# Kernel optimization log

Measured on AMD Instinct MI355X. Metric: run time of the kernel, lower is better.

The kernel has to match this reference:

```python
import jax, jax.numpy as jnp
import numpy as np

B, M, V, E, D, T = 512, 64, 20000, 1024, 384, 100
EPS = 1e-5


def setup_inputs() -> dict:
    key = jax.random.key(0)
    ks = jax.random.split(key, 26)
    w = lambda k, shape: (jax.random.normal(k, shape, jnp.float32) * 0.02)
    return {
        'x': jax.random.uniform(ks[0], (B, V), jnp.float32),
        'emb': jax.random.normal(ks[1], (B, M, D), jnp.float32),
        'lengths': jax.random.randint(ks[2], (B,), 1, M + 1, jnp.int32),
        'fc11_w': w(ks[3], (E, V)), 'fc11_b': jnp.zeros((E,), jnp.float32),
        'fc12_w': w(ks[4], (E, E)), 'fc12_b': jnp.zeros((E,), jnp.float32),
        'q_w': w(ks[5], (D, E)), 'q_b': jnp.zeros((D,), jnp.float32),
        'k_w': w(ks[6], (D, D)), 'k_b': jnp.zeros((D,), jnp.float32),
        'v_w': w(ks[7], (D, D)), 'v_b': jnp.zeros((D,), jnp.float32),
        'mean_w': w(ks[8], (T, D)), 'mean_b': jnp.zeros((T,), jnp.float32),
        'logvar_w': w(ks[9], (T, D)), 'logvar_b': jnp.zeros((T,), jnp.float32),
        'mean_bn_b': jnp.zeros((T,), jnp.float32),
        'logvar_bn_b': jnp.zeros((T,), jnp.float32),
        'dec_w': w(ks[10], (V, T)), 'dec_b': jnp.zeros((V,), jnp.float32),
        'dec_bn_b': jnp.zeros((V,), jnp.float32),
    }


def _bn(h, bias):
    # BatchNorm1d, training-mode batch stats, weight frozen at 1 (requires_grad=False)
    mu = h.mean(axis=0)
    var = h.var(axis=0)  # biased variance, as torch BN normalization
    return (h - mu) / jnp.sqrt(var + EPS) + bias


def reference(x, emb, lengths, fc11_w, fc11_b, fc12_w, fc12_b,
              q_w, q_b, k_w, k_b, v_w, v_b,
              mean_w, mean_b, logvar_w, logvar_b,
              mean_bn_b, logvar_bn_b, dec_w, dec_b, dec_bn_b):
    # encoder MLP (dropout p=0 -> identity)
    e1 = jax.nn.softplus(x @ fc11_w.T + fc11_b)
    h_bow = jax.nn.softplus(e1 @ fc12_w.T + fc12_b)  # [B, E]

    # ragged single-query attention over sentence embeddings, vectorized
    q = h_bow @ q_w.T + q_b                              # [B, D]
    k = jnp.einsum('bmd,ed->bme', emb, k_w) + k_b        # [B, M, D]
    v = jnp.einsum('bmd,ed->bme', emb, v_w) + v_b        # [B, M, D]
    scores = jnp.einsum('bd,bmd->bm', q, k) / jnp.sqrt(jnp.float32(D))
    valid = jnp.arange(M)[None, :] < lengths[:, None]    # [B, M]
    scores = jnp.where(valid, scores, -jnp.inf)
    alpha = jax.nn.softmax(scores, axis=-1)
    d_i = jnp.einsum('bm,bmd->bd', alpha, v)             # [B, D]

    mu = _bn(d_i @ mean_w.T + mean_b, mean_bn_b)         # [B, T]
    logvar = _bn(d_i @ logvar_w.T + logvar_b, logvar_bn_b)
    z = mu  # eval-mode reparameterize
    theta = jax.nn.softmax(z, axis=1)

    logit = theta @ dec_w.T + dec_b
    recon_log = jax.nn.log_softmax(_bn(logit, dec_bn_b), axis=-1)
    recon_loss = -(x * recon_log).sum(axis=1).mean()

    # KL prior: a = ones -> mu2 = 0, var2 = 1 - 1/T (scalar)
    var2 = 1.0 - 1.0 / T
    var = jnp.exp(logvar)
    kld = 0.5 * ((var / var2 + mu * mu / var2 + jnp.log(var2) - logvar).sum(axis=1) - T)
    loss_kl = kld.mean()
    return recon_loss + loss_kl
```

## Files before the change

kernel.cpp:

```cpp
#include <hip/hip_runtime.h>
#include <cstddef>

#define NB 512
#define NM 64
#define NV 20000
#define NE 1024
#define ND 384
#define NT 100
#define EPS 1e-5f

#define NVP 20096
#define NKP 128
#define NHS 256

typedef __bf16 bf16x8 __attribute__((ext_vector_type(8)));
typedef float f32x4 __attribute__((ext_vector_type(4)));

__device__ __forceinline__ float softplus_f(float x) {
    return fmaxf(x, 0.f) + log1pf(expf(-fabsf(x)));
}

__device__ __forceinline__ unsigned short f2bf(float f) {
    unsigned u = __builtin_bit_cast(unsigned, f);
    unsigned r = u + 0x7FFFu + ((u >> 16) & 1u);
    return (unsigned short)(r >> 16);
}

__device__ __forceinline__ float bf2f(unsigned short u) {
    return __builtin_bit_cast(float, (unsigned)u << 16);
}

__device__ __forceinline__ uint4 pack_bf8(float4 a, float4 b) {
    bf16x8 v;
    v[0] = (__bf16)a.x; v[1] = (__bf16)a.y; v[2] = (__bf16)a.z; v[3] = (__bf16)a.w;
    v[4] = (__bf16)b.x; v[5] = (__bf16)b.y; v[6] = (__bf16)b.z; v[7] = (__bf16)b.w;
    return __builtin_bit_cast(uint4, v);
}

__device__ __forceinline__ void convert8(const float* __restrict__ s,
                                         unsigned short* __restrict__ d,
                                         int b, int tid) {
    const size_t i = ((size_t)b * 256 + tid) * 8;
    const float4 a = *reinterpret_cast<const float4*>(s + i);
    const float4 c = *reinterpret_cast<const float4*>(s + i + 4);
    *reinterpret_cast<uint4*>(d + i) = pack_bf8(a, c);
}

#define PREP_C12 512
#define PREP_QW  192
#define PREP_VW  72
#define PREP_TR  144
#define PREP_HD  257
#define PREP_DW  (NVP / 2)
#define PREP_BLOCKS (PREP_C12 + PREP_QW + PREP_VW + PREP_TR + PREP_HD + PREP_DW)

__global__ __launch_bounds__(256) void prep_kernel(
        const float* __restrict__ fc12_w, unsigned short* __restrict__ w12b,
        const float* __restrict__ q_w,    unsigned short* __restrict__ qwb,
        const float* __restrict__ v_w,    unsigned short* __restrict__ vwb,
        const float* __restrict__ k_w,    unsigned short* __restrict__ kTb,
        const float* __restrict__ mw, const float* __restrict__ lw,
        const float* __restrict__ mb, const float* __restrict__ lb,
        unsigned short* __restrict__ headwb, float* __restrict__ headbb,
        const float* __restrict__ dec_w,  unsigned short* __restrict__ decwb) {
    __shared__ float tile[32][33];
    int b = blockIdx.x;
    const int tid = threadIdx.x;
    if (b < PREP_C12) { convert8(fc12_w, w12b, b, tid); return; }
    b -= PREP_C12;
    if (b < PREP_QW) { convert8(q_w, qwb, b, tid); return; }
    b -= PREP_QW;
    if (b < PREP_VW) { convert8(v_w, vwb, b, tid); return; }
    b -= PREP_VW;
    if (b < PREP_TR) {
        const int bx = (b % 12) * 32, by = (b / 12) * 32;
        const int tx = tid & 31, ty = tid >> 5;
        #pragma unroll
        for (int i = 0; i < 4; ++i)
            tile[ty + 8 * i][tx] = k_w[(size_t)(by + ty + 8 * i) * ND + bx + tx];
        __syncthreads();
        #pragma unroll
        for (int i = 0; i < 4; ++i)
            kTb[(size_t)(bx + ty + 8 * i) * ND + by + tx] = f2bf(tile[tx][ty + 8 * i]);
        return;
    }
    b -= PREP_TR;
    if (b < PREP_HD) {
        if (b == NHS) {
            if (tid < NHS)
                headbb[tid] = (tid < NT) ? mb[tid]
                            : (tid >= 128 && tid < 128 + NT) ? lb[tid - 128] : 0.f;
            return;
        }
        const float* src = (b < NT) ? (mw + (size_t)b * ND)
                         : (b >= 128 && b < 128 + NT) ? (lw + (size_t)(b - 128) * ND) : nullptr;
        for (int c = tid; c < ND; c += 256)
            headwb[(size_t)b * ND + c] = src ? f2bf(src[c]) : (unsigned short)0;
        return;
    }
    b -= PREP_HD;
    {
        const int n = b * 2 + (tid >> 7);
        const int k = tid & 127;
        decwb[(size_t)n * NKP + k] =
            (n < NV && k < NT) ? f2bf(dec_w[(size_t)n * NT + k]) : (unsigned short)0;
    }
}

#define BM 128
#define BN 128
#define BK 32

__global__ __launch_bounds__(256) void gemm_f32_splitk(
        const float* __restrict__ A,
        const float* __restrict__ Bw,
        unsigned short* __restrict__ partial,
        int M, int N, int K, int S, int steps_total, int gx, int gy) {
    __shared__ __align__(16) unsigned short Asl[BM * BK];
    __shared__ __align__(16) unsigned short Bsl[BN * BK];
    const int tid = threadIdx.x;
    const int l = blockIdx.x >> 3;
    const int xcd = blockIdx.x & 7;
    const int bm = l % gy;
    const int rest = l / gy;
    const int bn = rest % gx;
    const int s_loc = rest / gx;
    const int s = xcd * (S >> 3) + s_loc;

    const int row0 = bm * BM, col0 = bn * BN;
    const int k_begin = (int)(((long)s * steps_total) / S) * BK;
    const int k_end   = (int)(((long)(s + 1) * steps_total) / S) * BK;
    const int nsteps = (k_end - k_begin) / BK;

    const int sr = tid >> 2;
    const int sc = (tid & 3) * 8;
    const int wave = tid >> 6, lane = tid & 63;
    const int wm = wave >> 1, wn = wave & 1;
    const int lrow = lane & 15, lkb = lane >> 4;

    f32x4 acc[4][4] = {};
    const float* Ab = A + (size_t)row0 * K;
    const float* Bb = Bw + (size_t)col0 * K;

    float4 ra[2][2], rb[2][2];

#define LOADREGS(K0)                                                          \
    {                                                                         \
        _Pragma("unroll")                                                     \
        for (int h = 0; h < 2; ++h) {                                         \
            const float* pa = Ab + (size_t)(h * 64 + sr) * K + (K0) + sc;     \
            const float* pb = Bb + (size_t)(h * 64 + sr) * K + (K0) + sc;     \
            ra[h][0] = *reinterpret_cast<const float4*>(pa);                  \
            ra[h][1] = *reinterpret_cast<const float4*>(pa + 4);              \
            rb[h][0] = *reinterpret_cast<const float4*>(pb);                  \
            rb[h][1] = *reinterpret_cast<const float4*>(pb + 4);              \
        }                                                                     \
    }

#define WRITELDS()                                                            \
    {                                                                         \
        _Pragma("unroll")                                                     \
        for (int h = 0; h < 2; ++h) {                                         \
            *reinterpret_cast<uint4*>(&Asl[(h * 64 + sr) * BK + sc]) =        \
                pack_bf8(ra[h][0], ra[h][1]);                                 \
            *reinterpret_cast<uint4*>(&Bsl[(h * 64 + sr) * BK + sc]) =        \
                pack_bf8(rb[h][0], rb[h][1]);                                 \
        }                                                                     \
    }

    LOADREGS(k_begin);
    WRITELDS();
    __syncthreads();

    for (int t = 0; t < nsteps; ++t) {
        const bool has_next = (t + 1) < nsteps;
        if (has_next) LOADREGS(k_begin + (t + 1) * BK);

        bf16x8 af[4], bfr[4];
        #pragma unroll
        for (int i = 0; i < 4; ++i) {
            af[i]  = *reinterpret_cast<const bf16x8*>(&Asl[(wm * 64 + i * 16 + lrow) * BK + lkb * 8]);
            bfr[i] = *reinterpret_cast<const bf16x8*>(&Bsl[(wn * 64 + i * 16 + lrow) * BK + lkb * 8]);
        }
        #pragma unroll
        for (int i = 0; i < 4; ++i)
            #pragma unroll
            for (int j = 0; j < 4; ++j)
                acc[i][j] = __builtin_amdgcn_mfma_f32_16x16x32_bf16(af[i], bfr[j], acc[i][j], 0, 0, 0);

        __syncthreads();
        if (has_next) WRITELDS();
        __syncthreads();
    }
#undef LOADREGS
#undef WRITELDS

    unsigned short* P = partial + (size_t)s * M * N;
    #pragma unroll
    for (int i = 0; i < 4; ++i) {
        const int rbase = row0 + wm * 64 + i * 16 + lkb * 4;
        #pragma unroll
        for (int j = 0; j < 4; ++j) {
            const int col = col0 + wn * 64 + j * 16 + lrow;
            #pragma unroll
            for (int r = 0; r < 4; ++r)
                P[(size_t)(rbase + r) * N + col] = f2bf(acc[i][j][r]);
        }
    }
}

__global__ __launch_bounds__(256) void gemm_mfma_splitk(
        const unsigned short* __restrict__ A,
        const unsigned short* __restrict__ Bw,
        unsigned short* __restrict__ partial,
        int M, int N, int K, int S, int steps_total) {
    __shared__ __align__(16) unsigned short Asl[BM * BK];
    __shared__ __align__(16) unsigned short Bsl[BN * BK];
    const int tid = threadIdx.x;
    const int bn = blockIdx.x, bm = blockIdx.y, s = blockIdx.z;
    const int row0 = bm * BM, col0 = bn * BN;
    const int k_begin = (int)(((long)s * steps_total) / S) * BK;
    const int k_end   = (int)(((long)(s + 1) * steps_total) / S) * BK;

    const int srow = tid >> 2;
    const int scol = (tid & 3) * 8;
    const int wave = tid >> 6, lane = tid & 63;
    const int wm = wave >> 1, wn = wave & 1;
    const int lrow = lane & 15, lkb = lane >> 4;

    f32x4 acc[4][4] = {};
    const unsigned short* Ab = A + (size_t)row0 * K;
    const unsigned short* Bb = Bw + (size_t)col0 * K;

    for (int k0 = k_begin; k0 < k_end; k0 += BK) {
        #pragma unroll
        for (int i = 0; i < 2; ++i) {
            const int r = i * 64 + srow;
            __builtin_amdgcn_global_load_lds(
                (const __attribute__((address_space(1))) void*)(Ab + (size_t)r * K + k0 + scol),
                (__attribute__((address_space(3))) void*)(&Asl[(i * 256 + tid) * 8]),
                16, 0, 0);
            __builtin_amdgcn_global_load_lds(
                (const __attribute__((address_space(1))) void*)(Bb + (size_t)r * K + k0 + scol),
                (__attribute__((address_space(3))) void*)(&Bsl[(i * 256 + tid) * 8]),
                16, 0, 0);
        }
        __syncthreads();
        bf16x8 af[4], bfr[4];
        #pragma unroll
        for (int i = 0; i < 4; ++i) {
            af[i]  = *reinterpret_cast<const bf16x8*>(&Asl[(wm * 64 + i * 16 + lrow) * BK + lkb * 8]);
            bfr[i] = *reinterpret_cast<const bf16x8*>(&Bsl[(wn * 64 + i * 16 + lrow) * BK + lkb * 8]);
        }
        #pragma unroll
        for (int i = 0; i < 4; ++i)
            #pragma unroll
            for (int j = 0; j < 4; ++j)
                acc[i][j] = __builtin_amdgcn_mfma_f32_16x16x32_bf16(af[i], bfr[j], acc[i][j], 0, 0, 0);
        __syncthreads();
    }

    unsigned short* P = partial + (size_t)s * M * N;
    #pragma unroll
    for (int i = 0; i < 4; ++i) {
        const int rbase = row0 + wm * 64 + i * 16 + lkb * 4;
        #pragma unroll
        for (int j = 0; j < 4; ++j) {
            const int col = col0 + wn * 64 + j * 16 + lrow;
            #pragma unroll
            for (int r = 0; r < 4; ++r)
                P[(size_t)(rbase + r) * N + col] = f2bf(acc[i][j][r]);
        }
    }
}

__global__ __launch_bounds__(256) void gemm64_splitk(
        const unsigned short* __restrict__ A,
        const unsigned short* __restrict__ Bw,
        unsigned short* __restrict__ partial,
        int M, int N, int K, int S, int steps_total) {
    __shared__ __align__(16) unsigned short Asl[64 * BK];
    __shared__ __align__(16) unsigned short Bsl[64 * BK];
    const int tid = threadIdx.x;
    const int bn = blockIdx.x, bm = blockIdx.y, s = blockIdx.z;
    const int row0 = bm * 64, col0 = bn * 64;
    const int k_begin = (int)(((long)s * steps_total) / S) * BK;
    const int k_end   = (int)(((long)(s + 1) * steps_total) / S) * BK;

    const int srow = tid >> 2;
    const int scol = (tid & 3) * 8;
    const int wave = tid >> 6, lane = tid & 63;
    const int wm = wave >> 1, wn = wave & 1;
    const int lrow = lane & 15, lkb = lane >> 4;

    f32x4 acc[2][2] = {};
    const unsigned short* Ab = A + (size_t)row0 * K;
    const unsigned short* Bb = Bw + (size_t)col0 * K;

    for (int k0 = k_begin; k0 < k_end; k0 += BK) {
        __builtin_amdgcn_global_load_lds(
            (const __attribute__((address_space(1))) void*)(Ab + (size_t)srow * K + k0 + scol),
            (__attribute__((address_space(3))) void*)(&Asl[tid * 8]),
            16, 0, 0);
        __builtin_amdgcn_global_load_lds(
            (const __attribute__((address_space(1))) void*)(Bb + (size_t)srow * K + k0 + scol),
            (__attribute__((address_space(3))) void*)(&Bsl[tid * 8]),
            16, 0, 0);
        __syncthreads();
        bf16x8 af[2], bfr[2];
        #pragma unroll
        for (int i = 0; i < 2; ++i) {
            af[i]  = *reinterpret_cast<const bf16x8*>(&Asl[(wm * 32 + i * 16 + lrow) * BK + lkb * 8]);
            bfr[i] = *reinterpret_cast<const bf16x8*>(&Bsl[(wn * 32 + i * 16 + lrow) * BK + lkb * 8]);
        }
        #pragma unroll
        for (int i = 0; i < 2; ++i)
            #pragma unroll
            for (int j = 0; j < 2; ++j)
                acc[i][j] = __builtin_amdgcn_mfma_f32_16x16x32_bf16(af[i], bfr[j], acc[i][j], 0, 0, 0);
        __syncthreads();
    }

    unsigned short* P = partial + (size_t)s * M * N;
    #pragma unroll
    for (int i = 0; i < 2; ++i) {
        const int rbase = row0 + wm * 32 + i * 16 + lkb * 4;
        #pragma unroll
        for (int j = 0; j < 2; ++j) {
            const int col = col0 + wn * 32 + j * 16 + lrow;
            #pragma unroll
            for (int r = 0; r < 4; ++r)
                P[(size_t)(rbase + r) * N + col] = f2bf(acc[i][j][r]);
        }
    }
}

template<int OUT_BF16, int ACT, int HASBIAS>
__global__ __launch_bounds__(256) void reduce_splitk_bf(
        const unsigned short* __restrict__ partial,
        const float* __restrict__ bias,
        void* __restrict__ out, int MN, int N, int S) {
    const int i0 = (blockIdx.x * 256 + threadIdx.x) * 8;
    if (i0 >= MN) return;
    float sum[8] = {};
    for (int s = 0; s < S; ++s) {
        union { uint4 v; unsigned short u[8]; } p;
        p.v = *reinterpret_cast<const uint4*>(partial + (size_t)s * MN + i0);
        #pragma unroll
        for (int j = 0; j < 8; ++j) sum[j] += bf2f(p.u[j]);
    }
    if (HASBIAS) {
        const int nb = i0 % N;
        #pragma unroll
        for (int j = 0; j < 8; ++j) sum[j] += bias[nb + j];
    }
    if (ACT) {
        #pragma unroll
        for (int j = 0; j < 8; ++j) sum[j] = softplus_f(sum[j]);
    }
    if (OUT_BF16) {
        union { uint4 v; unsigned short u[8]; } r;
        #pragma unroll
        for (int j = 0; j < 8; ++j) r.u[j] = f2bf(sum[j]);
        *reinterpret_cast<uint4*>((unsigned short*)out + i0) = r.v;
    } else {
        float* o = (float*)out + i0;
        *reinterpret_cast<float4*>(o)     = make_float4(sum[0], sum[1], sum[2], sum[3]);
        *reinterpret_cast<float4*>(o + 4) = make_float4(sum[4], sum[5], sum[6], sum[7]);
    }
}

template<int OUT_BF16, int ACT, int HASBIAS, int COLSTATS>
__global__ __launch_bounds__(256) void gemm_mfma(
        const unsigned short* __restrict__ A,
        const unsigned short* __restrict__ Bw,
        const float* __restrict__ bias,
        void* __restrict__ Cout,
        float* __restrict__ colp,
        int M, int Nout, int K) {
    __shared__ __align__(16) unsigned short Asl[BM * BK];
    __shared__ __align__(16) unsigned short Bsl[BN * BK];
    const int tid = threadIdx.x;
    const int row0 = blockIdx.y * BM, col0 = blockIdx.x * BN;
    const int srow = tid >> 2;
    const int scol = (tid & 3) * 8;
    const int wave = tid >> 6, lane = tid & 63;
    const int wm = wave >> 1, wn = wave & 1;
    const int lrow = lane & 15, lkb = lane >> 4;

    f32x4 acc[4][4] = {};
    const unsigned short* Ab = A + (size_t)row0 * K;
    const unsigned short* Bb = Bw + (size_t)col0 * K;

    for (int k0 = 0; k0 < K; k0 += BK) {
        #pragma unroll
        for (int i = 0; i < 2; ++i) {
            const int r = i * 64 + srow;
            __builtin_amdgcn_global_load_lds(
                (const __attribute__((address_space(1))) void*)(Ab + (size_t)r * K + k0 + scol),
                (__attribute__((address_space(3))) void*)(&Asl[(i * 256 + tid) * 8]),
                16, 0, 0);
            __builtin_amdgcn_global_load_lds(
                (const __attribute__((address_space(1))) void*)(Bb + (size_t)r * K + k0 + scol),
                (__attribute__((address_space(3))) void*)(&Bsl[(i * 256 + tid) * 8]),
                16, 0, 0);
        }
        __syncthreads();
        bf16x8 af[4], bfr[4];
        #pragma unroll
        for (int i = 0; i < 4; ++i) {
            af[i]  = *reinterpret_cast<const bf16x8*>(&Asl[(wm * 64 + i * 16 + lrow) * BK + lkb * 8]);
            bfr[i] = *reinterpret_cast<const bf16x8*>(&Bsl[(wn * 64 + i * 16 + lrow) * BK + lkb * 8]);
        }
        #pragma unroll
        for (int i = 0; i < 4; ++i)
            #pragma unroll
            for (int j = 0; j < 4; ++j)
                acc[i][j] = __builtin_amdgcn_mfma_f32_16x16x32_bf16(af[i], bfr[j], acc[i][j], 0, 0, 0);
        __syncthreads();
    }

    #pragma unroll
    for (int j = 0; j < 4; ++j) {
        const int col = col0 + wn * 64 + j * 16 + lrow;
        const bool cok = col < Nout;
        const float bv = HASBIAS ? (cok ? bias[col] : 0.f) : 0.f;
        float csum = 0.f, csq = 0.f;
        #pragma unroll
        for (int i = 0; i < 4; ++i) {
            const int rbase = row0 + wm * 64 + i * 16 + lkb * 4;
            #pragma unroll
            for (int r = 0; r < 4; ++r) {
                float v = acc[i][j][r] + bv;
                if (ACT == 1) v = softplus_f(v);
                if (COLSTATS) { csum += v; csq = fmaf(v, v, csq); }
                if (cok) {
                    if (OUT_BF16)
                        ((unsigned short*)Cout)[(size_t)(rbase + r) * Nout + col] = f2bf(v);
                    else
                        ((float*)Cout)[(size_t)(rbase + r) * Nout + col] = v;
                }
            }
        }
        if (COLSTATS) {
            csum += __shfl_xor(csum, 16); csum += __shfl_xor(csum, 32);
            csq  += __shfl_xor(csq, 16);  csq  += __shfl_xor(csq, 32);
            if (lkb == 0) {
                const int w8 = blockIdx.y * 2 + wm;
                colp[(size_t)w8 * NVP + col] = csum;
                colp[(size_t)(8 + w8) * NVP + col] = csq;
            }
        }
    }
}

__global__ __launch_bounds__(256) void attn_kernel(const unsigned short* __restrict__ qkp,
                                                   const float* __restrict__ emb,
                                                   const int* __restrict__ lengths,
                                                   unsigned short* __restrict__ cb) {
    const int b = blockIdx.x;
    const int tid = threadIdx.x;
    __shared__ unsigned short es[NM * ND];
    __shared__ float qs[ND];
    __shared__ float sc[NM];

    const float* ebase = emb + (size_t)b * NM * ND;
    for (int i = tid; i < NM * ND / 8; i += 256) {
        const float4 v0 = *reinterpret_cast<const float4*>(ebase + (size_t)i * 8);
        const float4 v1 = *reinterpret_cast<const float4*>(ebase + (size_t)i * 8 + 4);
        *reinterpret_cast<uint4*>(&es[i * 8]) = pack_bf8(v0, v1);
    }
    for (int d = tid; d < ND; d += 256) {
        float acc = 0.f;
        #pragma unroll
        for (int s = 0; s < 8; ++s)
            acc += bf2f(qkp[((size_t)s * NB + b) * ND + d]);
        qs[d] = acc;
    }
    __syncthreads();

    const int wave = tid >> 6, lane = tid & 63;
    const float scale = 0.05103103630798288f;

    for (int m = wave; m < NM; m += 4) {
        float s = 0.f;
        for (int d = lane; d < ND; d += 64) s = fmaf(bf2f(es[m * ND + d]), qs[d], s);
        #pragma unroll
        for (int off = 32; off; off >>= 1) s += __shfl_xor(s, off);
        if (lane == 0) sc[m] = s * scale;
    }
    __syncthreads();

    const int len = lengths[b];
    if (tid < 64) {
        float s = (tid < len) ? sc[tid] : -INFINITY;
        float mx = s;
        #pragma unroll
        for (int off = 32; off; off >>= 1) mx = fmaxf(mx, __shfl_xor(mx, off));
        float e = (tid < len) ? expf(s - mx) : 0.f;
        float sum = e;
        #pragma unroll
        for (int off = 32; off; off >>= 1) sum += __shfl_xor(sum, off);
        sc[tid] = e / sum;
    }
    __syncthreads();

    for (int d = tid; d < ND; d += 256) {
        float acc = 0.f;
        for (int m = 0; m < len; ++m) acc = fmaf(sc[m], bf2f(es[m * ND + d]), acc);
        cb[(size_t)b * ND + d] = f2bf(acc);
    }
}

__global__ __launch_bounds__(256) void bn_batch(const float* __restrict__ hl,
                                                const float* __restrict__ mbnb,
                                                const float* __restrict__ lbnb,
                                                float* __restrict__ mu,
                                                float* __restrict__ lv) {
    const int t = blockIdx.x;
    const int sel = blockIdx.y;
    const int col = sel ? 128 + t : t;
    const float* bnb = sel ? lbnb : mbnb;
    float* dst = sel ? lv : mu;
    const int tid = threadIdx.x;

    float s = 0.f, ss = 0.f;
    for (int b = tid; b < NB; b += 256) {
        const float v = hl[(size_t)b * NHS + col];
        s += v; ss += v * v;
    }
    __shared__ float rs[256], rss[256];
    rs[tid] = s; rss[tid] = ss;
    __syncthreads();
    for (int off = 128; off; off >>= 1) {
        if (tid < off) { rs[tid] += rs[tid + off]; rss[tid] += rss[tid + off]; }
        __syncthreads();
    }
    const float mean = rs[0] / (float)NB;
    const float var = rss[0] / (float)NB - mean * mean;
    const float rstd = rsqrtf(var + EPS);
    const float bb = bnb[t];
    for (int b = tid; b < NB; b += 256) {
        dst[(size_t)b * NT + t] = (hl[(size_t)b * NHS + col] - mean) * rstd + bb;
    }
}

__global__ __launch_bounds__(128) void theta_kl(const float* __restrict__ mu,
                                                const float* __restrict__ lv,
                                                unsigned short* __restrict__ thetab,
                                                float* __restrict__ kld_p) {
    const int b = blockIdx.x, tid = threadIdx.x;
    const float var2 = 1.0f - 1.0f / (float)NT;
    const float inv_var2 = 1.0f / var2;
    __shared__ float red[128];

    const float m = (tid < NT) ? mu[(size_t)b * NT + tid] : -INFINITY;
    red[tid] = m;
    __syncthreads();
    for (int off = 64; off; off >>= 1) {
        if (tid < off) red[tid] = fmaxf(red[tid], red[tid + off]);
        __syncthreads();
    }
    const float mx = red[0];
    __syncthreads();

    const float e = (tid < NT) ? expf(m - mx) : 0.f;
    red[tid] = e;
    __syncthreads();
    for (int off = 64; off; off >>= 1) {
        if (tid < off) red[tid] += red[tid + off];
        __syncthreads();
    }
    const float sum = red[0];
    __syncthreads();
    thetab[(size_t)b * NKP + tid] = (tid < NT) ? f2bf(e / sum) : (unsigned short)0;

    float term = 0.f;
    if (tid < NT) {
        const float l = lv[(size_t)b * NT + tid];
        term = expf(l) * inv_var2 + m * m * inv_var2 - l;
    }
    red[tid] = term;
    __syncthreads();
    for (int off = 64; off; off >>= 1) {
        if (tid < off) red[tid] += red[tid + off];
        __syncthreads();
    }
    if (tid == 0)
        kld_p[b] = 0.5f * (red[0] + (float)NT * logf(var2) - (float)NT);
}

__global__ __launch_bounds__(256) void stats_final(const float* __restrict__ colp,
                                                   float* __restrict__ cmu,
                                                   float* __restrict__ crstd) {
    const int v = blockIdx.x * 256 + threadIdx.x;
    if (v >= NV) return;
    float s = 0.f, q = 0.f;
    #pragma unroll
    for (int w = 0; w < 8; ++w) {
        s += colp[(size_t)w * NVP + v];
        q += colp[(size_t)(8 + w) * NVP + v];
    }
    const float mean = s / (float)NB;
    cmu[v] = mean;
    crstd[v] = rsqrtf(q / (float)NB - mean * mean + EPS);
}

__global__ __launch_bounds__(256) void row_recon(const unsigned short* __restrict__ logitb,
                                                 const float* __restrict__ x,
                                                 const float* __restrict__ cmu,
                                                 const float* __restrict__ crstd,
                                                 const float* __restrict__ dbnb,
                                                 float* __restrict__ recon_p) {
    const int b = blockIdx.x, tid = threadIdx.x;
    const unsigned short* lr = logitb + (size_t)b * NV;
    const float* xr = x + (size_t)b * NV;

    float m_i = -INFINITY, s_i = 0.f, xz = 0.f, xs = 0.f;
    for (int v = tid * 8; v < NV; v += 2048) {
        union { uint4 v4; unsigned short u[8]; } lw;
        lw.v4 = *reinterpret_cast<const uint4*>(lr + v);
        const float4 x0 = *reinterpret_cast<const float4*>(xr + v);
        const float4 x1 = *reinterpret_cast<const float4*>(xr + v + 4);
        const float4 c0 = *reinterpret_cast<const float4*>(cmu + v);
        const float4 c1 = *reinterpret_cast<const float4*>(cmu + v + 4);
        const float4 r0 = *reinterpret_cast<const float4*>(crstd + v);
        const float4 r1 = *reinterpret_cast<const float4*>(crstd + v + 4);
        const float4 d0 = *reinterpret_cast<const float4*>(dbnb + v);
        const float4 d1 = *reinterpret_cast<const float4*>(dbnb + v + 4);
        const float xv[8] = {x0.x,x0.y,x0.z,x0.w,x1.x,x1.y,x1.z,x1.w};
        const float cm[8] = {c0.x,c0.y,c0.z,c0.w,c1.x,c1.y,c1.z,c1.w};
        const float cr[8] = {r0.x,r0.y,r0.z,r0.w,r1.x,r1.y,r1.z,r1.w};
        const float db[8] = {d0.x,d0.y,d0.z,d0.w,d1.x,d1.y,d1.z,d1.w};
        float z[8];
        #pragma unroll
        for (int j = 0; j < 8; ++j)
            z[j] = fmaf(bf2f(lw.u[j]) - cm[j], cr[j], db[j]);
        float mx = z[0];
        #pragma unroll
        for (int j = 1; j < 8; ++j) mx = fmaxf(mx, z[j]);
        const float mnew = fmaxf(m_i, mx);
        float e8 = 0.f;
        #pragma unroll
        for (int j = 0; j < 8; ++j) e8 += expf(z[j] - mnew);
        s_i = s_i * expf(m_i - mnew) + e8;
        m_i = mnew;
        #pragma unroll
        for (int j = 0; j < 8; ++j) {
            xz = fmaf(xv[j], z[j], xz);
            xs += xv[j];
        }
    }

    __shared__ float rm[256], rs[256], rxz[256], rxs[256];
    rm[tid] = m_i; rs[tid] = s_i; rxz[tid] = xz; rxs[tid] = xs;
    __syncthreads();
    for (int off = 128; off; off >>= 1) {
        if (tid < off) {
            const float m1 = rm[tid], m2 = rm[tid + off];
            const float s1 = rs[tid], s2 = rs[tid + off];
            const float mm = fmaxf(m1, m2);
            rm[tid] = mm;
            rs[tid] = s1 * expf(m1 - mm) + s2 * expf(m2 - mm);
            rxz[tid] += rxz[tid + off];
            rxs[tid] += rxs[tid + off];
        }
        __syncthreads();
    }
    if (tid == 0) {
        const float lse = rm[0] + logf(rs[0]);
        recon_p[b] = rxz[0] - lse * rxs[0];
    }
}

__global__ __launch_bounds__(512) void finalize(const float* __restrict__ recon_p,
                                                const float* __restrict__ kld_p,
                                                float* __restrict__ out) {
    const int tid = threadIdx.x;
    __shared__ float r1[512], r2[512];
    r1[tid] = recon_p[tid];
    r2[tid] = kld_p[tid];
    __syncthreads();
    for (int off = 256; off; off >>= 1) {
        if (tid < off) { r1[tid] += r1[tid + off]; r2[tid] += r2[tid + off]; }
        __syncthreads();
    }
    if (tid == 0) out[0] = (-r1[0] + r2[0]) / (float)NB;
}

extern "C" void kernel_launch(void* const* d_in, const int* in_sizes, int n_in,
                              void* d_out, int out_size, void* d_ws, size_t ws_size,
                              hipStream_t stream) {
    const float* x       = (const float*)d_in[0];
    const float* emb     = (const float*)d_in[1];
    const int*   lengths = (const int*)d_in[2];
    const float* fc11_w  = (const float*)d_in[3];
    const float* fc11_b  = (const float*)d_in[4];
    const float* fc12_w  = (const float*)d_in[5];
    const float* fc12_b  = (const float*)d_in[6];
    const float* q_w     = (const float*)d_in[7];
    const float* q_b     = (const float*)d_in[8];
    const float* k_w     = (const float*)d_in[9];
    const float* v_w     = (const float*)d_in[11];
    const float* v_b     = (const float*)d_in[12];
    const float* mean_w  = (const float*)d_in[13];
    const float* mean_b  = (const float*)d_in[14];
    const float* lvw     = (const float*)d_in[15];
    const float* lvb     = (const float*)d_in[16];
    const float* mbnb    = (const float*)d_in[17];
    const float* lbnb    = (const float*)d_in[18];
    const float* dec_w   = (const float*)d_in[19];
    const float* dec_b   = (const float*)d_in[20];
    const float* dbnb    = (const float*)d_in[21];
    float* out = (float*)d_out;

    char* base = (char*)d_ws;
    size_t off = 0;
    auto alloc = [&](size_t bytes) -> void* {
        void* p = base + off;
        off += (bytes + 255) & ~(size_t)255;
        return p;
    };

    unsigned short* logitb = (unsigned short*)alloc((size_t)NB * NV * 2);
    unsigned short* w12b   = (unsigned short*)alloc((size_t)NE * NE * 2);
    unsigned short* e1b    = (unsigned short*)alloc((size_t)NB * NE * 2);
    unsigned short* hb     = (unsigned short*)alloc((size_t)NB * NE * 2);
    unsigned short* qwb    = (unsigned short*)alloc((size_t)ND * NE * 2);
    unsigned short* kTb    = (unsigned short*)alloc((size_t)ND * ND * 2);
    unsigned short* vwb    = (unsigned short*)alloc((size_t)ND * ND * 2);
    unsigned short* qb     = (unsigned short*)alloc((size_t)NB * ND * 2);
    unsigned short* cb     = (unsigned short*)alloc((size_t)NB * ND * 2);
    unsigned short* dib    = (unsigned short*)alloc((size_t)NB * ND * 2);
    unsigned short* headwb = (unsigned short*)alloc((size_t)NHS * ND * 2);
    float*          headbb = (float*)alloc((size_t)NHS * 4);
    float*          hl     = (float*)alloc((size_t)NB * NHS * 4);
    float*          mu     = (float*)alloc((size_t)NB * NT * 4);
    float*          lv     = (float*)alloc((size_t)NB * NT * 4);
    float*          colp   = (float*)alloc((size_t)16 * NVP * 4);
    float*          cmu    = (float*)alloc((size_t)NV * 4);
    float*          crstd  = (float*)alloc((size_t)NV * 4);
    float*          rp     = (float*)alloc((size_t)NB * 4);
    float*          kp     = (float*)alloc((size_t)NB * 4);
    unsigned short* decwb  = (unsigned short*)alloc((size_t)NVP * NKP * 2);
    unsigned short* thetab = (unsigned short*)alloc((size_t)NB * NKP * 2);
    unsigned short* smallp = (unsigned short*)alloc((size_t)16 * NB * ND * 2);
    const size_t part_bytes_per_s = ((size_t)NB * NE * 2 + 255) & ~(size_t)255;
    const size_t remain = (ws_size > off) ? (ws_size - off) : 0;
    const int S11 = (remain >= 32 * part_bytes_per_s) ? 32
                  : (remain >= 16 * part_bytes_per_s) ? 16 : 8;
    unsigned short* partb = (unsigned short*)alloc((size_t)S11 * NB * NE * 2);

    const dim3 blk(256);

    prep_kernel<<<PREP_BLOCKS, blk, 0, stream>>>(
        fc12_w, w12b, q_w, qwb, v_w, vwb, k_w, kTb,
        mean_w, lvw, mean_b, lvb, headwb, headbb, dec_w, decwb);

    gemm_f32_splitk<<<(NE / BN) * (NB / BM) * S11, blk, 0, stream>>>(
        x, fc11_w, partb, NB, NE, NV, S11, NV / BK, NE / BN, NB / BM);
    reduce_splitk_bf<1, 1, 1><<<(NB * NE) / 2048, blk, 0, stream>>>(
        partb, fc11_b, e1b, NB * NE, NE, S11);

    gemm_mfma_splitk<<<dim3(NE / BN, NB / BM, 8), blk, 0, stream>>>(
        e1b, w12b, partb, NB, NE, NE, 8, NE / BK);
    reduce_splitk_bf<1, 1, 1><<<(NB * NE) / 2048, blk, 0, stream>>>(
        partb, fc12_b, hb, NB * NE, NE, 8);

    gemm64_splitk<<<dim3(ND / 64, NB / 64, 16), blk, 0, stream>>>(
        hb, qwb, smallp, NB, ND, NE, 16, NE / BK);
    reduce_splitk_bf<1, 0, 1><<<(NB * ND) / 2048, blk, 0, stream>>>(
        smallp, q_b, qb, NB * ND, ND, 16);
    gemm64_splitk<<<dim3(ND / 64, NB / 64, 8), blk, 0, stream>>>(
        qb, kTb, smallp, NB, ND, ND, 8, ND / BK);
    attn_kernel<<<NB, 256, 0, stream>>>(smallp, emb, lengths, cb);
    gemm64_splitk<<<dim3(ND / 64, NB / 64, 8), blk, 0, stream>>>(
        cb, vwb, smallp, NB, ND, ND, 8, ND / BK);
    reduce_splitk_bf<1, 0, 1><<<(NB * ND) / 2048, blk, 0, stream>>>(
        smallp, v_b, dib, NB * ND, ND, 8);
    gemm64_splitk<<<dim3(NHS / 64, NB / 64, 8), blk, 0, stream>>>(
        dib, headwb, smallp, NB, NHS, ND, 8, ND / BK);
    reduce_splitk_bf<0, 0, 1><<<(NB * NHS) / 2048, blk, 0, stream>>>(
        smallp, headbb, hl, NB * NHS, NHS, 8);
    bn_batch<<<dim3(NT, 2), blk, 0, stream>>>(hl, mbnb, lbnb, mu, lv);
    theta_kl<<<NB, 128, 0, stream>>>(mu, lv, thetab, kp);
    gemm_mfma<1, 0, 1, 1><<<dim3(NVP / BN, NB / BM), blk, 0, stream>>>(
        thetab, decwb, dec_b, logitb, colp, NB, NV, NKP);
    stats_final<<<(NV + 255) / 256, blk, 0, stream>>>(colp, cmu, crstd);
    row_recon<<<NB, 256, 0, stream>>>(logitb, x, cmu, crstd, dbnb, rp);
    finalize<<<1, 512, 0, stream>>>(rp, kp, out);
}
```

Baseline: 181.3 us.

## Use 256x256 tiles with swizzled LDS for the fp32 fc11 split-K GEMM

Replaces the 128x128-tile fp32-input split-K GEMM for fc11 with a 512-thread, 256x256-tile kernel. Each wave now computes a 128x64 sub-tile, and LDS rows use an XOR swizzle to avoid bank conflicts. The larger tile halves the number of re-reads of x and fc11_w from global memory, but each thread holds more accumulator registers and there are fewer blocks, which can lower occupancy. The logit buffer now aliases the split-K partial buffer to save workspace, so more configurations can use a higher split count.

```diff
diff --git a/kernel.cpp b/kernel.cpp
--- a/kernel.cpp
+++ b/kernel.cpp
@@ -111,61 +111,61 @@
 #define BN 128
 #define BK 32
 
-__global__ __launch_bounds__(256) void gemm_f32_splitk(
+__device__ __forceinline__ int lds_off(int row, int slot) {
+    return row * BK + ((slot ^ ((row >> 1) & 3)) << 3);
+}
+
+__global__ __launch_bounds__(512, 2) void gemm_f32_256(
         const float* __restrict__ A,
         const float* __restrict__ Bw,
         unsigned short* __restrict__ partial,
-        int M, int N, int K, int S, int steps_total, int gx, int gy) {
-    __shared__ __align__(16) unsigned short Asl[BM * BK];
-    __shared__ __align__(16) unsigned short Bsl[BN * BK];
+        int M, int N, int K, int S, int steps_total) {
+    __shared__ __align__(16) unsigned short Asl[256 * BK];
+    __shared__ __align__(16) unsigned short Bsl[256 * BK];
     const int tid = threadIdx.x;
+    const int xcd = blockIdx.x & 7;
     const int l = blockIdx.x >> 3;
-    const int xcd = blockIdx.x & 7;
-    const int bm = l % gy;
-    const int rest = l / gy;
-    const int bn = rest % gx;
-    const int s_loc = rest / gx;
-    const int s = xcd * (S >> 3) + s_loc;
-
-    const int row0 = bm * BM, col0 = bn * BN;
+    const int tile = l & 7;
+    const int s = xcd + 8 * (l >> 3);
+    const int bm = tile & 1, bn = tile >> 1;
+    const int row0 = bm * 256, col0 = bn * 256;
     const int k_begin = (int)(((long)s * steps_total) / S) * BK;
     const int k_end   = (int)(((long)(s + 1) * steps_total) / S) * BK;
     const int nsteps = (k_end - k_begin) / BK;
 
-    const int sr = tid >> 2;
-    const int sc = (tid & 3) * 8;
+    const int sr = tid >> 1;
+    const int sc = (tid & 1) * 16;
+    const int sslot = (tid & 1) * 2;
     const int wave = tid >> 6, lane = tid & 63;
-    const int wm = wave >> 1, wn = wave & 1;
+    const int wm = wave >> 2, wn = wave & 3;
     const int lrow = lane & 15, lkb = lane >> 4;
 
-    f32x4 acc[4][4] = {};
+    f32x4 acc[8][4] = {};
     const float* Ab = A + (size_t)row0 * K;
     const float* Bb = Bw + (size_t)col0 * K;
 
-    float4 ra[2][2], rb[2][2];
+    float4 ra[4], rb[4];
 
 #define LOADREGS(K0)                                                          \
     {                                                                         \
-        _Pragma("unroll")                                                     \
-        for (int h = 0; h < 2; ++h) {                                         \
-            const float* pa = Ab + (size_t)(h * 64 + sr) * K + (K0) + sc;     \
-            const float* pb = Bb + (size_t)(h * 64 + sr) * K + (K0) + sc;     \
-            ra[h][0] = *reinterpret_cast<const float4*>(pa);                  \
-            ra[h][1] = *reinterpret_cast<const float4*>(pa + 4);              \
-            rb[h][0] = *reinterpret_cast<const float4*>(pb);                  \
-            rb[h][1] = *reinterpret_cast<const float4*>(pb + 4);              \
-        }                                                                     \
+        const float* pa = Ab + (size_t)sr * K + (K0) + sc;                    \
+        const float* pb = Bb + (size_t)sr * K + (K0) + sc;                    \
+        ra[0] = *reinterpret_cast<const float4*>(pa);                         \
+        ra[1] = *reinterpret_cast<const float4*>(pa + 4);                     \
+        ra[2] = *reinterpret_cast<const float4*>(pa + 8);                     \
+        ra[3] = *reinterpret_cast<const float4*>(pa + 12);                    \
+        rb[0] = *reinterpret_cast<const float4*>(pb);                         \
+        rb[1] = *reinterpret_cast<const float4*>(pb + 4);                     \
+        rb[2] = *reinterpret_cast<const float4*>(pb + 8);                     \
+        rb[3] = *reinterpret_cast<const float4*>(pb + 12);                    \
     }
 
 #define WRITELDS()                                                            \
     {                                                                         \
-        _Pragma("unroll")                                                     \
-        for (int h = 0; h < 2; ++h) {                                         \
-            *reinterpret_cast<uint4*>(&Asl[(h * 64 + sr) * BK + sc]) =        \
-                pack_bf8(ra[h][0], ra[h][1]);                                 \
-            *reinterpret_cast<uint4*>(&Bsl[(h * 64 + sr) * BK + sc]) =        \
-                pack_bf8(rb[h][0], rb[h][1]);                                 \
-        }                                                                     \
+        *reinterpret_cast<uint4*>(&Asl[lds_off(sr, sslot)])     = pack_bf8(ra[0], ra[1]); \
+        *reinterpret_cast<uint4*>(&Asl[lds_off(sr, sslot + 1)]) = pack_bf8(ra[2], ra[3]); \
+        *reinterpret_cast<uint4*>(&Bsl[lds_off(sr, sslot)])     = pack_bf8(rb[0], rb[1]); \
+        *reinterpret_cast<uint4*>(&Bsl[lds_off(sr, sslot + 1)]) = pack_bf8(rb[2], rb[3]); \
     }
 
     LOADREGS(k_begin);
@@ -176,14 +176,15 @@
         const bool has_next = (t + 1) < nsteps;
         if (has_next) LOADREGS(k_begin + (t + 1) * BK);
 
-        bf16x8 af[4], bfr[4];
-        #pragma unroll
-        for (int i = 0; i < 4; ++i) {
-            af[i]  = *reinterpret_cast<const bf16x8*>(&Asl[(wm * 64 + i * 16 + lrow) * BK + lkb * 8]);
-            bfr[i] = *reinterpret_cast<const bf16x8*>(&Bsl[(wn * 64 + i * 16 + lrow) * BK + lkb * 8]);
-        }
-        #pragma unroll
-        for (int i = 0; i < 4; ++i)
+        bf16x8 af[8], bfr[4];
+        #pragma unroll
+        for (int i = 0; i < 8; ++i)
+            af[i] = *reinterpret_cast<const bf16x8*>(&Asl[lds_off(wm * 128 + i * 16 + lrow, lkb)]);
+        #pragma unroll
+        for (int j = 0; j < 4; ++j)
+            bfr[j] = *reinterpret_cast<const bf16x8*>(&Bsl[lds_off(wn * 64 + j * 16 + lrow, lkb)]);
+        #pragma unroll
+        for (int i = 0; i < 8; ++i)
             #pragma unroll
             for (int j = 0; j < 4; ++j)
                 acc[i][j] = __builtin_amdgcn_mfma_f32_16x16x32_bf16(af[i], bfr[j], acc[i][j], 0, 0, 0);
@@ -197,8 +198,8 @@
 
     unsigned short* P = partial + (size_t)s * M * N;
     #pragma unroll
-    for (int i = 0; i < 4; ++i) {
-        const int rbase = row0 + wm * 64 + i * 16 + lkb * 4;
+    for (int i = 0; i < 8; ++i) {
+        const int rbase = row0 + wm * 128 + i * 16 + lkb * 4;
         #pragma unroll
         for (int j = 0; j < 4; ++j) {
             const int col = col0 + wn * 64 + j * 16 + lrow;
@@ -722,7 +723,6 @@
         return p;
     };
 
-    unsigned short* logitb = (unsigned short*)alloc((size_t)NB * NV * 2);
     unsigned short* w12b   = (unsigned short*)alloc((size_t)NE * NE * 2);
     unsigned short* e1b    = (unsigned short*)alloc((size_t)NB * NE * 2);
     unsigned short* hb     = (unsigned short*)alloc((size_t)NB * NE * 2);
@@ -745,11 +745,15 @@
     unsigned short* decwb  = (unsigned short*)alloc((size_t)NVP * NKP * 2);
     unsigned short* thetab = (unsigned short*)alloc((size_t)NB * NKP * 2);
     unsigned short* smallp = (unsigned short*)alloc((size_t)16 * NB * ND * 2);
-    const size_t part_bytes_per_s = ((size_t)NB * NE * 2 + 255) & ~(size_t)255;
+    const size_t part_per_s = (size_t)NB * NE * 2;
+    const size_t logit_bytes = (size_t)NB * NV * 2;
     const size_t remain = (ws_size > off) ? (ws_size - off) : 0;
-    const int S11 = (remain >= 32 * part_bytes_per_s) ? 32
-                  : (remain >= 16 * part_bytes_per_s) ? 16 : 8;
-    unsigned short* partb = (unsigned short*)alloc((size_t)S11 * NB * NE * 2);
+    const int S11 = (remain >= 32 * part_per_s) ? 32
+                  : (remain >= 16 * part_per_s + logit_bytes) ? 16 : 8;
+    size_t part_alloc = S11 * part_per_s;
+    if (part_alloc < logit_bytes) part_alloc = logit_bytes;
+    unsigned short* partb = (unsigned short*)alloc(part_alloc);
+    unsigned short* logitb = partb;
 
     const dim3 blk(256);
 
@@ -757,8 +761,8 @@
         fc12_w, w12b, q_w, qwb, v_w, vwb, k_w, kTb,
         mean_w, lvw, mean_b, lvb, headwb, headbb, dec_w, decwb);
 
-    gemm_f32_splitk<<<(NE / BN) * (NB / BM) * S11, blk, 0, stream>>>(
-        x, fc11_w, partb, NB, NE, NV, S11, NV / BK, NE / BN, NB / BM);
+    gemm_f32_256<<<8 * S11, 512, 0, stream>>>(
+        x, fc11_w, partb, NB, NE, NV, S11, NV / BK);
     reduce_splitk_bf<1, 1, 1><<<(NB * NE) / 2048, blk, 0, stream>>>(
         partb, fc11_b, e1b, NB * NE, NE, S11);
 
```

New measurement: 167.5 us. -7.6%, faster.
